# Performance work log

Hardware: AMD Instinct MI355X
Metric: run time of the kernel (lower is better)

Reference implementation:

```python
import jax, jax.numpy as jnp
import numpy as np

B, S, E, H = 2, 2048, 512, 8
DH = E // H
SCALE = DH ** -0.5
TEMPERATURE = 1.0
LN_EPS = 1e-5


def setup_inputs() -> dict:
    key = jax.random.key(0)
    ks = jax.random.split(key, 12)
    s = E ** -0.5
    return {
        "q": jax.random.normal(ks[0], (B, S, E), jnp.float32),
        "k": jax.random.normal(ks[1], (B, S, E), jnp.float32),
        "v": jax.random.normal(ks[2], (B, S, E), jnp.float32),
        "Wq": jax.random.normal(ks[3], (E, E), jnp.float32) * s,
        "bq": jnp.zeros((E,), jnp.float32),
        "Wk": jax.random.normal(ks[4], (E, E), jnp.float32) * s,
        "bk": jnp.zeros((E,), jnp.float32),
        "Wv": jax.random.normal(ks[5], (E, E), jnp.float32) * s,
        "bv": jnp.zeros((E,), jnp.float32),
        "Wo": jax.random.normal(ks[6], (E, E), jnp.float32) * s,
        "bo": jnp.zeros((E,), jnp.float32),
        "ln_g": jnp.ones((E,), jnp.float32),
        "ln_b": jnp.zeros((E,), jnp.float32),
    }


def reference(q, k, v, Wq, bq, Wk, bk, Wv, bv, Wo, bo, ln_g, ln_b):
    # QKV projections (nn.Linear: x @ W.T + b)
    qh = (q @ Wq.T + bq).reshape(B, S, H, DH).transpose(0, 2, 1, 3)  # [B,H,S,Dh]
    kh = (k @ Wk.T + bk).reshape(B, S, H, DH).transpose(0, 2, 1, 3)
    vh = (v @ Wv.T + bv).reshape(B, S, H, DH).transpose(0, 2, 1, 3)
    # attention scores [B,H,S,S], scaled then divided by temperature
    scores = jnp.einsum('bhqd,bhkd->bhqk', qh, kh) * (SCALE / TEMPERATURE)
    attn = jax.nn.softmax(scores, axis=-1)
    # dropout is identity in eval mode
    x = jnp.einsum('bhqk,bhkd->bhqd', attn, vh)  # [B,H,S,Dh]
    x = x.transpose(0, 2, 1, 3).reshape(B, S, E)
    # out projection + LayerNorm
    y = x @ Wo.T + bo
    mu = jnp.mean(y, axis=-1, keepdims=True)
    var = jnp.var(y, axis=-1, keepdims=True)
    out = (y - mu) * jax.lax.rsqrt(var + LN_EPS) * ln_g + ln_b
    return out
```

## Files before the change

kernel.cpp:

```cpp
#include <hip/hip_runtime.h>
#include <hip/hip_bf16.h>
#include <stdint.h>

#define B_ 2
#define S_ 2048
#define E_ 512
#define H_ 8
#define DH_ 64
#define BH_ (B_*H_)
#define M_ (B_*S_)

typedef short short8 __attribute__((ext_vector_type(8)));
typedef float f32x4 __attribute__((ext_vector_type(4)));
typedef float f32x16 __attribute__((ext_vector_type(16)));
typedef int int4v __attribute__((ext_vector_type(4)));

#define QSCALE 0.18033688011112042f

#if __has_builtin(__builtin_amdgcn_exp2f)
#define EXP2(x) __builtin_amdgcn_exp2f(x)
#else
#define EXP2(x) exp2f(x)
#endif

__device__ __forceinline__ float asf(uint32_t u) { return __builtin_bit_cast(float, u); }
__device__ __forceinline__ uint32_t asu(float f) { return __builtin_bit_cast(uint32_t, f); }

__device__ __forceinline__ ushort f2bf(float f) {
  uint32_t u = __builtin_bit_cast(uint32_t, f);
  u += 0x7fffu + ((u >> 16) & 1u);
  return (ushort)(u >> 16);
}

__device__ __forceinline__ uint32_t cvtpk(float lo, float hi) {
  uint32_t r;
  asm("v_cvt_pk_bf16_f32 %0, %1, %2" : "=v"(r) : "v"(lo), "v"(hi));
  return r;
}

__device__ __forceinline__ void swap32(uint32_t a, uint32_t b, uint32_t& o0, uint32_t& o1) {
#if __has_builtin(__builtin_amdgcn_permlane32_swap)
  typedef int v2i __attribute__((ext_vector_type(2)));
  v2i r = __builtin_amdgcn_permlane32_swap((int)a, (int)b, false, false);
  o0 = (uint32_t)r.x; o1 = (uint32_t)r.y;
#else
  int laneid = (int)(threadIdx.x & 63);
  uint32_t pa = (uint32_t)__shfl_xor((int)a, 32, 64);
  uint32_t pb = (uint32_t)__shfl_xor((int)b, 32, 64);
  bool hi = laneid >= 32;
  o0 = hi ? pb : a;
  o1 = hi ? b : pa;
#endif
}

__device__ __forceinline__ void gll16(const void* g, void* l) {
  __builtin_amdgcn_global_load_lds((const __attribute__((address_space(1))) void*)g,
                                   (__attribute__((address_space(3))) void*)l,
                                   16, 0, 0);
}

struct CvtArgs {
  const float* s[7];
  ushort* d[7];
  int nq[7];
};

__global__ __launch_bounds__(256) void cvt_kernel(CvtArgs a) {
  int seg = blockIdx.y;
  int i = blockIdx.x * 256 + threadIdx.x;
  if (i >= a.nq[seg]) return;
  float4 v = ((const float4*)a.s[seg])[i];
  ushort4 o;
  o.x = f2bf(v.x); o.y = f2bf(v.y); o.z = f2bf(v.z); o.w = f2bf(v.w);
  ((ushort4*)a.d[seg])[i] = o;
}

template<int EPI>
__global__ __launch_bounds__(256) void gemm_bt(
    const ushort* __restrict__ A0, const ushort* __restrict__ A1, const ushort* __restrict__ A2,
    const ushort* __restrict__ W0, const ushort* __restrict__ W1, const ushort* __restrict__ W2,
    const float* __restrict__ bias0, const float* __restrict__ bias1, const float* __restrict__ bias2,
    ushort* O0, ushort* O1, ushort* O2, float* Yout)
{
  const int K = E_;
  int z = blockIdx.z;
  const ushort* A = (z == 0) ? A0 : ((z == 1) ? A1 : A2);
  const ushort* W = (z == 0) ? W0 : ((z == 1) ? W1 : W2);
  const float* bias = (z == 0) ? bias0 : ((z == 1) ? bias1 : bias2);
  ushort* O = (z == 0) ? O0 : ((z == 1) ? O1 : O2);
  float scale = (EPI == 0 && z == 0) ? QSCALE : 1.0f;

  int n0 = blockIdx.x * 128, m0 = blockIdx.y * 128;
  int tid = threadIdx.x, lane = tid & 63, wid = tid >> 6;
  int wm = wid >> 1, wn = wid & 1;

  __shared__ ushort As[128 * 32];
  __shared__ ushort Bs[128 * 32];

  f32x4 acc[4][4];
#pragma unroll
  for (int i = 0; i < 4; ++i)
#pragma unroll
    for (int j = 0; j < 4; ++j)
      acc[i][j] = (f32x4){0.f, 0.f, 0.f, 0.f};

  for (int kt = 0; kt < K / 32; ++kt) {
    int k0 = kt * 32;
#pragma unroll
    for (int c = 0; c < 2; ++c) {
      int f = c * 256 + tid;
      int r = f >> 2;
      int lc = (f & 3) ^ ((r >> 1) & 3);
      gll16(A + (m0 + r) * K + k0 + lc * 8, (char*)As + (c * 256 + wid * 64) * 16);
    }
#pragma unroll
    for (int c = 0; c < 2; ++c) {
      int f = c * 256 + tid;
      int r = f >> 2;
      int lc = (f & 3) ^ ((r >> 1) & 3);
      gll16(W + (n0 + r) * K + k0 + lc * 8, (char*)Bs + (c * 256 + wid * 64) * 16);
    }
    __syncthreads();

    short8 af[4], bf[4];
#pragma unroll
    for (int fm = 0; fm < 4; ++fm) {
      int r = wm * 64 + fm * 16 + (lane & 15);
      int phys = (lane >> 4) ^ ((r >> 1) & 3);
      af[fm] = *(const short8*)((const char*)As + r * 64 + phys * 16);
    }
#pragma unroll
    for (int fn = 0; fn < 4; ++fn) {
      int r = wn * 64 + fn * 16 + (lane & 15);
      int phys = (lane >> 4) ^ ((r >> 1) & 3);
      bf[fn] = *(const short8*)((const char*)Bs + r * 64 + phys * 16);
    }
#pragma unroll
    for (int fm = 0; fm < 4; ++fm)
#pragma unroll
      for (int fn = 0; fn < 4; ++fn)
        acc[fm][fn] = __builtin_amdgcn_mfma_f32_16x16x32_bf16(af[fm], bf[fn], acc[fm][fn], 0, 0, 0);
    __syncthreads();
  }

#pragma unroll
  for (int fm = 0; fm < 4; ++fm) {
#pragma unroll
    for (int fn = 0; fn < 4; ++fn) {
#pragma unroll
      for (int j = 0; j < 4; ++j) {
        int m = m0 + wm * 64 + fm * 16 + (lane >> 4) * 4 + j;
        int n = n0 + wn * 64 + fn * 16 + (lane & 15);
        float v = (acc[fm][fn][j] + bias[n]) * scale;
        if constexpr (EPI == 0) {
          int b = m >> 11, s = m & (S_ - 1);
          int h = n >> 6, d = n & 63;
          O[((b * H_ + h) * S_ + s) * DH_ + d] = f2bf(v);
        } else {
          Yout[m * E_ + n] = v;
        }
      }
    }
  }
}

__global__ __launch_bounds__(256) void vtrans(const ushort* __restrict__ Vh, ushort* __restrict__ Vt) {
  int bh = blockIdx.y;
  int s0 = blockIdx.x * 64;
  __shared__ ushort t[64][72];
  int tid = threadIdx.x;
  const ushort* src = Vh + ((size_t)bh * S_ + s0) * DH_;
  int r = tid >> 2, c0 = (tid & 3) * 16;
#pragma unroll
  for (int i = 0; i < 2; ++i) {
    short8 v = *(const short8*)(src + r * DH_ + c0 + i * 8);
#pragma unroll
    for (int kx = 0; kx < 8; ++kx) t[r][c0 + i * 8 + kx] = (ushort)v[kx];
  }
  __syncthreads();
  int d = tid >> 2, j0 = (tid & 3) * 16;
  ushort* dst = Vt + ((size_t)bh * DH_ + d) * S_ + s0 + j0;
#pragma unroll
  for (int i = 0; i < 2; ++i) {
    short8 o;
#pragma unroll
    for (int kx = 0; kx < 8; ++kx) o[kx] = (short)t[j0 + i * 8 + kx][d];
    *(short8*)(dst + i * 8) = o;
  }
}

__global__ __launch_bounds__(256, 2) void attn_kernel(const ushort* __restrict__ Qh,
                                                      const ushort* __restrict__ Kh,
                                                      const ushort* __restrict__ Vt,
                                                      ushort* __restrict__ X) {
  int bh = blockIdx.x;
  int q0 = blockIdx.y * 64;
  int tid = threadIdx.x, lane = tid & 63, wid = tid >> 6;
  int wq = wid & 1, wk = wid >> 1;
  int hi = lane >> 5;

  __shared__ ushort lds_[32768];
  char* L = (char*)lds_;

  const ushort* Kg = Kh + (size_t)bh * S_ * DH_;
  const ushort* Vg = Vt + (size_t)bh * DH_ * S_;

  int q = q0 + wq * 32 + (lane & 31);
  const ushort* Qrow = Qh + ((size_t)bh * S_ + q) * DH_;
  short8 qf[4];
#pragma unroll
  for (int ds = 0; ds < 4; ++ds)
    qf[ds] = *(const short8*)(Qrow + ds * 16 + hi * 8);

  f32x16 sacc[2], oacc[2];
#pragma unroll
  for (int r = 0; r < 16; ++r) { oacc[0][r] = 0.f; oacc[1][r] = 0.f; }
  float m_r = -INFINITY, l_r = 0.f;

  const int NT = 16;

#define STAGE(buf, t)                                                          \
  do {                                                                         \
    int kb0 = (t) * 64, kb1 = 1024 + (t) * 64;                                 \
    _Pragma("unroll")                                                          \
    for (int w2 = 0; w2 < 2; ++w2) {                                           \
      int kb = w2 ? kb1 : kb0;                                                 \
      char* Kd = L + (buf) * 32768 + w2 * 16384;                               \
      char* Vd = Kd + 8192;                                                    \
      _Pragma("unroll")                                                        \
      for (int c = 0; c < 2; ++c) {                                            \
        int f = c * 256 + tid;                                                 \
        int r = f >> 3;                                                        \
        int lc = (f & 7) ^ (r & 7);                                            \
        gll16(Kg + (size_t)(kb + r) * DH_ + lc * 8, Kd + (c * 256 + wid * 64) * 16); \
        gll16(Vg + (size_t)r * S_ + kb + lc * 8, Vd + (c * 256 + wid * 64) * 16);    \
      }                                                                        \
    }                                                                          \
  } while (0)

  STAGE(0, 0);
  __syncthreads();

  for (int t = 0; t < NT; ++t) {
    int cur = t & 1;
    if (t + 1 < NT) STAGE(cur ^ 1, t + 1);

    const char* Kt = L + cur * 32768 + wk * 16384;
    const char* Vtile = Kt + 8192;

#pragma unroll
    for (int c = 0; c < 2; ++c) {
#pragma unroll
      for (int r = 0; r < 16; ++r) sacc[c][r] = 0.f;
      int kl = c * 32 + (lane & 31);
#pragma unroll
      for (int ds = 0; ds < 4; ++ds) {
        short8 kf = *(const short8*)(Kt + kl * 128 + (((2 * ds + hi) ^ (kl & 7)) * 16));
        sacc[c] = __builtin_amdgcn_mfma_f32_32x32x16_bf16(kf, qf[ds], sacc[c], 0, 0, 0);
      }
    }

    float mx = sacc[0][0];
#pragma unroll
    for (int r = 1; r < 16; ++r) mx = fmaxf(mx, sacc[0][r]);
#pragma unroll
    for (int r = 0; r < 16; ++r) mx = fmaxf(mx, sacc[1][r]);
    {
      uint32_t e0, e1;
      swap32(asu(mx), asu(mx), e0, e1);
      mx = fmaxf(asf(e0), asf(e1));
    }
    float mnew = fmaxf(m_r, mx);
    float scf = EXP2(m_r - mnew);
    m_r = mnew;
    float rs = 0.f;
#pragma unroll
    for (int c = 0; c < 2; ++c)
#pragma unroll
      for (int r = 0; r < 16; ++r) {
        float p = EXP2(sacc[c][r] - mnew);
        sacc[c][r] = p;
        rs += p;
      }
    {
      uint32_t e0, e1;
      swap32(asu(rs), asu(rs), e0, e1);
      rs = asf(e0) + asf(e1);
    }
    l_r = l_r * scf + rs;
#pragma unroll
    for (int dblk = 0; dblk < 2; ++dblk)
#pragma unroll
      for (int r = 0; r < 16; ++r) oacc[dblk][r] *= scf;

    uint32_t w[2][8];
#pragma unroll
    for (int c = 0; c < 2; ++c)
#pragma unroll
      for (int i = 0; i < 8; ++i)
        w[c][i] = cvtpk(sacc[c][2 * i], sacc[c][2 * i + 1]);

    short8 pf[4];
#pragma unroll
    for (int ks = 0; ks < 4; ++ks) {
      int c = ks >> 1, j = ks & 1;
      uint32_t e01, e45, e23, e67;
      swap32(w[c][4 * j + 0], w[c][4 * j + 2], e01, e45);
      swap32(w[c][4 * j + 1], w[c][4 * j + 3], e23, e67);
      int4v iv;
      iv[0] = (int)e01; iv[1] = (int)e23; iv[2] = (int)e45; iv[3] = (int)e67;
      pf[ks] = __builtin_bit_cast(short8, iv);
    }

#pragma unroll
    for (int ks = 0; ks < 4; ++ks) {
      int dl0 = (lane & 31);
#pragma unroll
      for (int dblk = 0; dblk < 2; ++dblk) {
        int dl = dblk * 32 + dl0;
        short8 vf = *(const short8*)(Vtile + dl * 128 + (((2 * ks + hi) ^ (dl & 7)) * 16));
        oacc[dblk] = __builtin_amdgcn_mfma_f32_32x32x16_bf16(vf, pf[ks], oacc[dblk], 0, 0, 0);
      }
    }

    __syncthreads();
  }
#undef STAGE

  float* fl = (float*)L;
  if (wk == 1) {
#pragma unroll
    for (int dblk = 0; dblk < 2; ++dblk)
#pragma unroll
      for (int r = 0; r < 16; ++r)
        fl[((wq * 2 + dblk) * 16 + r) * 64 + lane] = oacc[dblk][r];
    fl[4096 + wq * 64 + lane] = m_r;
    fl[4224 + wq * 64 + lane] = l_r;
  }
  __syncthreads();
  if (wk == 0) {
    float m1 = fl[4096 + wq * 64 + lane];
    float l1 = fl[4224 + wq * 64 + lane];
    float mstar = fmaxf(m_r, m1);
    float a0 = EXP2(m_r - mstar);
    float a1 = EXP2(m1 - mstar);
    float lstar = l_r * a0 + l1 * a1;
    float invl = 1.0f / lstar;
    int b = bh >> 3, h = bh & 7;
    int s = q0 + wq * 32 + (lane & 31);
    ushort* Xrow = X + (size_t)(b * S_ + s) * E_ + h * DH_;
#pragma unroll
    for (int dblk = 0; dblk < 2; ++dblk) {
#pragma unroll
      for (int i = 0; i < 8; ++i) {
        int r0 = 2 * i, r1 = 2 * i + 1;
        float o0 = (oacc[dblk][r0] * a0 + fl[((wq * 2 + dblk) * 16 + r0) * 64 + lane] * a1) * invl;
        float o1 = (oacc[dblk][r1] * a0 + fl[((wq * 2 + dblk) * 16 + r1) * 64 + lane] * a1) * invl;
        int d = dblk * 32 + (r0 & 3) + 8 * (r0 >> 2) + 4 * hi;
        *(uint32_t*)(Xrow + d) = cvtpk(o0, o1);
      }
    }
  }
}

__global__ __launch_bounds__(256) void ln_kernel(const float* __restrict__ Y,
                                                 const float* __restrict__ g,
                                                 const float* __restrict__ bta,
                                                 float* __restrict__ out) {
  int tid = threadIdx.x, lane = tid & 63, wid = tid >> 6;
  int row = blockIdx.x * 4 + wid;
  const float* y = Y + (size_t)row * E_;
  float4 v0 = *(const float4*)(y + lane * 8);
  float4 v1 = *(const float4*)(y + lane * 8 + 4);
  float s = v0.x + v0.y + v0.z + v0.w + v1.x + v1.y + v1.z + v1.w;
  float q = v0.x * v0.x + v0.y * v0.y + v0.z * v0.z + v0.w * v0.w +
            v1.x * v1.x + v1.y * v1.y + v1.z * v1.z + v1.w * v1.w;
#pragma unroll
  for (int msk = 1; msk < 64; msk <<= 1) {
    s += __shfl_xor(s, msk);
    q += __shfl_xor(q, msk);
  }
  float mu = s * (1.f / E_);
  float var = q * (1.f / E_) - mu * mu;
  float inv = rsqrtf(var + 1e-5f);
  float4 g0 = *(const float4*)(g + lane * 8);
  float4 g1 = *(const float4*)(g + lane * 8 + 4);
  float4 b0 = *(const float4*)(bta + lane * 8);
  float4 b1 = *(const float4*)(bta + lane * 8 + 4);
  float4 o0, o1;
  o0.x = (v0.x - mu) * inv * g0.x + b0.x;
  o0.y = (v0.y - mu) * inv * g0.y + b0.y;
  o0.z = (v0.z - mu) * inv * g0.z + b0.z;
  o0.w = (v0.w - mu) * inv * g0.w + b0.w;
  o1.x = (v1.x - mu) * inv * g1.x + b1.x;
  o1.y = (v1.y - mu) * inv * g1.y + b1.y;
  o1.z = (v1.z - mu) * inv * g1.z + b1.z;
  o1.w = (v1.w - mu) * inv * g1.w + b1.w;
  float* op = out + (size_t)row * E_;
  *(float4*)(op + lane * 8) = o0;
  *(float4*)(op + lane * 8 + 4) = o1;
}

extern "C" void kernel_launch(void* const* d_in, const int* in_sizes, int n_in,
                              void* d_out, int out_size, void* d_ws, size_t ws_size,
                              hipStream_t stream) {
  const float* q = (const float*)d_in[0];
  const float* k = (const float*)d_in[1];
  const float* v = (const float*)d_in[2];
  const float* Wq = (const float*)d_in[3];
  const float* bq = (const float*)d_in[4];
  const float* Wk = (const float*)d_in[5];
  const float* bk = (const float*)d_in[6];
  const float* Wv = (const float*)d_in[7];
  const float* bv = (const float*)d_in[8];
  const float* Wo = (const float*)d_in[9];
  const float* bo = (const float*)d_in[10];
  const float* ln_g = (const float*)d_in[11];
  const float* ln_b = (const float*)d_in[12];

  char* ws = (char*)d_ws;
  const size_t MB = 1024 * 1024;
  ushort* qb  = (ushort*)(ws + 0 * MB);
  ushort* kb  = (ushort*)(ws + 4 * MB);
  ushort* vb  = (ushort*)(ws + 8 * MB);
  ushort* Wqb = (ushort*)(ws + 12 * MB);
  ushort* Wkb = (ushort*)(ws + 12 * MB + 512 * 1024);
  ushort* Wvb = (ushort*)(ws + 13 * MB);
  ushort* Wob = (ushort*)(ws + 13 * MB + 512 * 1024);
  ushort* Qhb = (ushort*)(ws + 14 * MB);
  ushort* Khb = (ushort*)(ws + 18 * MB);
  ushort* Vhb = (ushort*)(ws + 22 * MB);
  ushort* Vtb = (ushort*)(ws + 26 * MB);
  ushort* Xb  = (ushort*)(ws + 30 * MB);
  float*  Yb  = (float*)(ws + 34 * MB);

  CvtArgs ca;
  ca.s[0] = q;  ca.d[0] = qb;  ca.nq[0] = (B_ * S_ * E_) / 4;
  ca.s[1] = k;  ca.d[1] = kb;  ca.nq[1] = (B_ * S_ * E_) / 4;
  ca.s[2] = v;  ca.d[2] = vb;  ca.nq[2] = (B_ * S_ * E_) / 4;
  ca.s[3] = Wq; ca.d[3] = Wqb; ca.nq[3] = (E_ * E_) / 4;
  ca.s[4] = Wk; ca.d[4] = Wkb; ca.nq[4] = (E_ * E_) / 4;
  ca.s[5] = Wv; ca.d[5] = Wvb; ca.nq[5] = (E_ * E_) / 4;
  ca.s[6] = Wo; ca.d[6] = Wob; ca.nq[6] = (E_ * E_) / 4;

  cvt_kernel<<<dim3(2048, 7), dim3(256), 0, stream>>>(ca);

  gemm_bt<0><<<dim3(4, 32, 3), dim3(256), 0, stream>>>(
      qb, kb, vb, Wqb, Wkb, Wvb, bq, bk, bv, Qhb, Khb, Vhb, (float*)nullptr);

  vtrans<<<dim3(S_ / 64, BH_), dim3(256), 0, stream>>>(Vhb, Vtb);

  attn_kernel<<<dim3(BH_, S_ / 64), dim3(256), 0, stream>>>(Qhb, Khb, Vtb, Xb);

  gemm_bt<1><<<dim3(4, 32, 1), dim3(256), 0, stream>>>(
      Xb, Xb, Xb, Wob, Wob, Wob, bo, bo, bo,
      (ushort*)nullptr, (ushort*)nullptr, (ushort*)nullptr, Yb);

  ln_kernel<<<dim3(M_ / 4), dim3(256), 0, stream>>>(Yb, ln_g, ln_b, (float*)d_out);
}
```

Measured before the change: 77.54 us.

## Halve attention key tile to 32 and raise occupancy with lazy softmax rescale

The attention kernel now processes 32 keys per wave per iteration instead of 64. This halves LDS usage and register accumulators, and launch bounds are raised to allow 4 blocks per CU. The V tile staging layout is reworked to match the smaller tile. It also adds a lazy rescale: the running max and output rescaling are skipped when all lanes' new max exceeds the old by at most 8 in the log2 domain. The cost is twice as many iterations and barriers, plus a risk of reduced precision or overflow headroom from the lazy max threshold.

```diff
diff --git a/kernel.cpp b/kernel.cpp
--- a/kernel.cpp
+++ b/kernel.cpp
@@ -189,7 +189,7 @@
   }
 }
 
-__global__ __launch_bounds__(256, 2) void attn_kernel(const ushort* __restrict__ Qh,
+__global__ __launch_bounds__(256, 4) void attn_kernel(const ushort* __restrict__ Qh,
                                                       const ushort* __restrict__ Kh,
                                                       const ushort* __restrict__ Vt,
                                                       ushort* __restrict__ X) {
@@ -199,7 +199,7 @@
   int wq = wid & 1, wk = wid >> 1;
   int hi = lane >> 5;
 
-  __shared__ ushort lds_[32768];
+  __shared__ ushort lds_[16384];
   char* L = (char*)lds_;
 
   const ushort* Kg = Kh + (size_t)bh * S_ * DH_;
@@ -212,28 +212,28 @@
   for (int ds = 0; ds < 4; ++ds)
     qf[ds] = *(const short8*)(Qrow + ds * 16 + hi * 8);
 
-  f32x16 sacc[2], oacc[2];
+  f32x16 sacc, oacc[2];
 #pragma unroll
   for (int r = 0; r < 16; ++r) { oacc[0][r] = 0.f; oacc[1][r] = 0.f; }
   float m_r = -INFINITY, l_r = 0.f;
 
-  const int NT = 16;
+  const int NT = 32;
 
 #define STAGE(buf, t)                                                          \
   do {                                                                         \
-    int kb0 = (t) * 64, kb1 = 1024 + (t) * 64;                                 \
     _Pragma("unroll")                                                          \
     for (int w2 = 0; w2 < 2; ++w2) {                                           \
-      int kb = w2 ? kb1 : kb0;                                                 \
-      char* Kd = L + (buf) * 32768 + w2 * 16384;                               \
-      char* Vd = Kd + 8192;                                                    \
-      _Pragma("unroll")                                                        \
-      for (int c = 0; c < 2; ++c) {                                            \
-        int f = c * 256 + tid;                                                 \
-        int r = f >> 3;                                                        \
-        int lc = (f & 7) ^ (r & 7);                                            \
-        gll16(Kg + (size_t)(kb + r) * DH_ + lc * 8, Kd + (c * 256 + wid * 64) * 16); \
-        gll16(Vg + (size_t)r * S_ + kb + lc * 8, Vd + (c * 256 + wid * 64) * 16);    \
+      int kb = w2 * 1024 + (t) * 32;                                           \
+      char* Kd = L + (buf) * 16384 + w2 * 8192;                                \
+      char* Vd = Kd + 4096;                                                    \
+      {                                                                        \
+        int r = tid >> 3, lc = (tid & 7) ^ (r & 7);                            \
+        gll16(Kg + (size_t)(kb + r) * DH_ + lc * 8, Kd + wid * 1024);          \
+      }                                                                        \
+      {                                                                        \
+        int rho = tid >> 3, l2 = (tid & 7) ^ (rho & 7);                        \
+        int d = rho + ((l2 >> 2) << 5), kc = (l2 & 3) * 8;                     \
+        gll16(Vg + (size_t)d * S_ + kb + kc, Vd + wid * 1024);                 \
       }                                                                        \
     }                                                                          \
   } while (0)
@@ -245,80 +245,75 @@
     int cur = t & 1;
     if (t + 1 < NT) STAGE(cur ^ 1, t + 1);
 
-    const char* Kt = L + cur * 32768 + wk * 16384;
-    const char* Vtile = Kt + 8192;
-
-#pragma unroll
-    for (int c = 0; c < 2; ++c) {
-#pragma unroll
-      for (int r = 0; r < 16; ++r) sacc[c][r] = 0.f;
-      int kl = c * 32 + (lane & 31);
-#pragma unroll
-      for (int ds = 0; ds < 4; ++ds) {
-        short8 kf = *(const short8*)(Kt + kl * 128 + (((2 * ds + hi) ^ (kl & 7)) * 16));
-        sacc[c] = __builtin_amdgcn_mfma_f32_32x32x16_bf16(kf, qf[ds], sacc[c], 0, 0, 0);
-      }
-    }
-
-    float mx = sacc[0][0];
-#pragma unroll
-    for (int r = 1; r < 16; ++r) mx = fmaxf(mx, sacc[0][r]);
-#pragma unroll
-    for (int r = 0; r < 16; ++r) mx = fmaxf(mx, sacc[1][r]);
-    {
+    const char* Kt = L + cur * 16384 + wk * 8192;
+    const char* Vtile = Kt + 4096;
+
+#pragma unroll
+    for (int r = 0; r < 16; ++r) sacc[r] = 0.f;
+    int kl = lane & 31;
+#pragma unroll
+    for (int ds = 0; ds < 4; ++ds) {
+      short8 kf = *(const short8*)(Kt + kl * 128 + (((2 * ds + hi) ^ (kl & 7)) * 16));
+      sacc = __builtin_amdgcn_mfma_f32_32x32x16_bf16(kf, qf[ds], sacc, 0, 0, 0);
+    }
+
+    float mx = fmaxf(fmaxf(sacc[0], sacc[1]), sacc[2]);
+    mx = fmaxf(mx, fmaxf(fmaxf(sacc[3], sacc[4]), sacc[5]));
+    mx = fmaxf(mx, fmaxf(fmaxf(sacc[6], sacc[7]), sacc[8]));
+    mx = fmaxf(mx, fmaxf(fmaxf(sacc[9], sacc[10]), sacc[11]));
+    mx = fmaxf(mx, fmaxf(fmaxf(sacc[12], sacc[13]), sacc[14]));
+    mx = fmaxf(mx, sacc[15]);
+    bool skip = __all(mx - m_r <= 8.0f);
+    if (!skip) {
       uint32_t e0, e1;
       swap32(asu(mx), asu(mx), e0, e1);
-      mx = fmaxf(asf(e0), asf(e1));
-    }
-    float mnew = fmaxf(m_r, mx);
-    float scf = EXP2(m_r - mnew);
-    m_r = mnew;
-    float rs = 0.f;
-#pragma unroll
-    for (int c = 0; c < 2; ++c)
-#pragma unroll
-      for (int r = 0; r < 16; ++r) {
-        float p = EXP2(sacc[c][r] - mnew);
-        sacc[c][r] = p;
-        rs += p;
-      }
+      float mnew = fmaxf(m_r, fmaxf(asf(e0), asf(e1)));
+      float scf = EXP2(m_r - mnew);
+      m_r = mnew;
+      l_r *= scf;
+#pragma unroll
+      for (int dblk = 0; dblk < 2; ++dblk)
+#pragma unroll
+        for (int r = 0; r < 16; ++r) oacc[dblk][r] *= scf;
+    }
+    float rs0 = 0.f, rs1 = 0.f;
+#pragma unroll
+    for (int r = 0; r < 16; r += 2) {
+      float p0 = EXP2(sacc[r] - m_r);
+      float p1 = EXP2(sacc[r + 1] - m_r);
+      sacc[r] = p0; sacc[r + 1] = p1;
+      rs0 += p0; rs1 += p1;
+    }
+    float rs = rs0 + rs1;
     {
       uint32_t e0, e1;
       swap32(asu(rs), asu(rs), e0, e1);
-      rs = asf(e0) + asf(e1);
-    }
-    l_r = l_r * scf + rs;
-#pragma unroll
-    for (int dblk = 0; dblk < 2; ++dblk)
-#pragma unroll
-      for (int r = 0; r < 16; ++r) oacc[dblk][r] *= scf;
-
-    uint32_t w[2][8];
-#pragma unroll
-    for (int c = 0; c < 2; ++c)
-#pragma unroll
-      for (int i = 0; i < 8; ++i)
-        w[c][i] = cvtpk(sacc[c][2 * i], sacc[c][2 * i + 1]);
-
-    short8 pf[4];
-#pragma unroll
-    for (int ks = 0; ks < 4; ++ks) {
-      int c = ks >> 1, j = ks & 1;
+      l_r += asf(e0) + asf(e1);
+    }
+
+    uint32_t w[8];
+#pragma unroll
+    for (int i = 0; i < 8; ++i)
+      w[i] = cvtpk(sacc[2 * i], sacc[2 * i + 1]);
+
+    short8 pf[2];
+#pragma unroll
+    for (int ks = 0; ks < 2; ++ks) {
       uint32_t e01, e45, e23, e67;
-      swap32(w[c][4 * j + 0], w[c][4 * j + 2], e01, e45);
-      swap32(w[c][4 * j + 1], w[c][4 * j + 3], e23, e67);
+      swap32(w[4 * ks + 0], w[4 * ks + 2], e01, e45);
+      swap32(w[4 * ks + 1], w[4 * ks + 3], e23, e67);
       int4v iv;
       iv[0] = (int)e01; iv[1] = (int)e23; iv[2] = (int)e45; iv[3] = (int)e67;
       pf[ks] = __builtin_bit_cast(short8, iv);
     }
 
 #pragma unroll
-    for (int ks = 0; ks < 4; ++ks) {
-      int dl0 = (lane & 31);
+    for (int ks = 0; ks < 2; ++ks) {
+      int rho = lane & 31;
 #pragma unroll
       for (int dblk = 0; dblk < 2; ++dblk) {
-        int dl = dblk * 32 + dl0;
-        short8 vf = *(const short8*)(Vtile + dl * 128 + (((2 * ks + hi) ^ (dl & 7)) * 16));
+        int lch = dblk * 4 + 2 * ks + hi;
+        short8 vf = *(const short8*)(Vtile + rho * 128 + ((lch ^ (rho & 7)) * 16));
         oacc[dblk] = __builtin_amdgcn_mfma_f32_32x32x16_bf16(vf, pf[ks], oacc[dblk], 0, 0, 0);
       }
     }
```

Result: no change. 77.65 us (+0.1%).
